# Optimization experiments

Hardware: AMD Instinct MI355X
Metric: run time of the kernel (lower is better)

Reference implementation:

```python
import jax, jax.numpy as jnp
import numpy as np

N_NODES = 200000
N_DEST = 8192
N_EDGE = 262144
E_TOTAL = 1000000
D_MEM = 128
D_FEAT = 128
D_EDGE = 64
D_TIME = 32
D_READ = 128
D_MSG = 128
D_AGG = 128
D_UPD = 128


def _glorot(key, shape):
    fan_in = shape[0]
    return jax.random.normal(key, shape, dtype=jnp.float32) * (1.0 / np.sqrt(fan_in))


def setup_inputs() -> dict:
    key = jax.random.key(0)
    ks = jax.random.split(key, 16)
    inp = {
        "node_memory": jax.random.normal(ks[0], (N_NODES, D_MEM), dtype=jnp.float32),
        "node_features": jax.random.normal(ks[1], (N_NODES, D_FEAT), dtype=jnp.float32),
        "edge_features": jax.random.normal(ks[2], (E_TOTAL, D_EDGE), dtype=jnp.float32),
        "time_encoding": jax.random.normal(ks[3], (N_EDGE, D_TIME), dtype=jnp.float32),
        "node_ids": jnp.arange(N_DEST, dtype=jnp.int64),
        "source_ids": jax.random.randint(ks[4], (N_EDGE,), 0, N_NODES, dtype=jnp.int64),
        "edge_ids": jax.random.randint(ks[5], (N_EDGE,), 0, E_TOTAL, dtype=jnp.int64),
        "dest_seg": jnp.sort(jax.random.randint(ks[6], (N_EDGE,), 0, N_DEST, dtype=jnp.int64)),
        # learned parameters
        "W_read": _glorot(ks[7], (D_MEM + D_FEAT, D_READ)),
        "b_read": jnp.zeros((D_READ,), dtype=jnp.float32),
        "W_msg": _glorot(ks[8], (D_READ + D_EDGE + D_TIME, D_MSG)),
        "b_msg": jnp.zeros((D_MSG,), dtype=jnp.float32),
        "W_agg": _glorot(ks[9], (D_READ + D_MSG, D_AGG)),
        "b_agg": jnp.zeros((D_AGG,), dtype=jnp.float32),
        "W_upd": _glorot(ks[10], (D_AGG + D_READ, D_UPD)),
        "b_upd": jnp.zeros((D_UPD,), dtype=jnp.float32),
        "W_write": _glorot(ks[11], (D_UPD, D_MEM)),
        "b_write": jnp.zeros((D_MEM,), dtype=jnp.float32),
    }
    return inp


def reference(node_memory, node_features, edge_features, time_encoding,
              node_ids, source_ids, edge_ids, dest_seg,
              W_read, b_read, W_msg, b_msg, W_agg, b_agg,
              W_upd, b_upd, W_write, b_write):
    n_dest = node_ids.shape[0]
    # source memory readout: gather + fuse(mem, feat) -> linear -> relu
    src_in = jnp.concatenate([node_memory[source_ids], node_features[source_ids]], axis=-1)
    src_read = jax.nn.relu(src_in @ W_read + b_read)                       # [E, D_READ]
    # message builder: fuse(source readout, edge feats, time enc) -> linear -> relu
    msg_in = jnp.concatenate([src_read, edge_features[edge_ids], time_encoding], axis=-1)
    msgs = jax.nn.relu(msg_in @ W_msg + b_msg)                             # [E, D_MSG]
    # ragged per-destination mean aggregation (replaces torch.split groups)
    msg_sum = jax.ops.segment_sum(msgs, dest_seg, num_segments=n_dest)     # [n_dest, D_MSG]
    cnt = jax.ops.segment_sum(jnp.ones((msgs.shape[0], 1), msgs.dtype), dest_seg, num_segments=n_dest)
    msg_mean = msg_sum / jnp.maximum(cnt, 1.0)
    # destination memory readout (shared with source readout: dest config is None)
    dst_in = jnp.concatenate([node_memory[node_ids], node_features[node_ids]], axis=-1)
    dst_read = jax.nn.relu(dst_in @ W_read + b_read)                       # [n_dest, D_READ]
    # aggregator: fuse(dest readout, mean messages) -> linear -> relu
    agg = jax.nn.relu(jnp.concatenate([dst_read, msg_mean], axis=-1) @ W_agg + b_agg)
    # memory updater: fuse(agg, dest readout) -> linear -> relu
    upd = jax.nn.relu(jnp.concatenate([agg, dst_read], axis=-1) @ W_upd + b_upd)
    # write-in: linear -> tanh, scatter back into node_memory
    write = jnp.tanh(upd @ W_write + b_write)                              # [n_dest, D_MEM]
    return node_memory.at[node_ids].set(write)
```

## Files before the change

kernel.cpp:

```cpp
#include <hip/hip_runtime.h>
#include <hip/hip_bf16.h>


typedef __bf16 bf16_t;
typedef __bf16 bf16x4 __attribute__((ext_vector_type(4)));
typedef __bf16 bf16x8 __attribute__((ext_vector_type(8)));
typedef float  f32x4  __attribute__((ext_vector_type(4)));

#define NNODES 200000
#define NDEST  8192
#define NEDGE  262144

__global__ void pack_weights_kernel(const float* __restrict__ Wr, const float* __restrict__ Wm,
                                    const float* __restrict__ Wa, const float* __restrict__ Wu,
                                    const float* __restrict__ Ww,
                                    bf16_t* __restrict__ Pr, bf16_t* __restrict__ Pm,
                                    bf16_t* __restrict__ Pa, bf16_t* __restrict__ Pu,
                                    bf16_t* __restrict__ Pw) {
    int p = blockIdx.x * 256 + threadIdx.x;
    const float* src; bf16_t* dst; int rel;
    if (p < 32768)       { src = Wr; dst = Pr; rel = p; }
    else if (p < 61440)  { src = Wm; dst = Pm; rel = p - 32768; }
    else if (p < 94208)  { src = Wa; dst = Pa; rel = p - 61440; }
    else if (p < 126976) { src = Wu; dst = Pu; rel = p - 94208; }
    else if (p < 143360) { src = Ww; dst = Pw; rel = p - 126976; }
    else return;
    int j    = rel & 7;
    int lane = (rel >> 3) & 63;
    int t    = rel >> 9;
    int nb   = t & 7;
    int kb   = t >> 3;
    int row  = kb * 32 + ((lane >> 4) << 3) + j;
    int col  = nb * 16 + (lane & 15);
    dst[rel] = (bf16_t)src[row * 128 + col];
}

__global__ __launch_bounds__(256, 2) void edge_kernel(
    const float* __restrict__ node_memory, const float* __restrict__ node_features,
    const float* __restrict__ edge_features, const float* __restrict__ time_enc,
    const int* __restrict__ source_ids, const int* __restrict__ edge_ids,
    const int* __restrict__ dest_seg,
    const bf16_t* __restrict__ Pr, const bf16_t* __restrict__ Pm,
    const float* __restrict__ b_read, const float* __restrict__ b_msg,
    float* __restrict__ msg_sum, float* __restrict__ out) {

    __shared__ __align__(16) bf16_t A1[64 * 264];
    __shared__ __align__(16) bf16_t A2[64 * 232];
    __shared__ int s_src[64], s_dst[64], s_eid[64];

    const int tid = threadIdx.x;
    const int e0  = blockIdx.x * 64;

    if (tid < 64) {
        s_src[tid] = source_ids[e0 + tid];
        s_dst[tid] = dest_seg[e0 + tid];
        s_eid[tid] = edge_ids[e0 + tid];
    }
    __syncthreads();

    #pragma unroll
    for (int i = 0; i < 16; ++i) {
        int c  = i * 256 + tid;
        int m  = c >> 6;
        int kc = (c & 63) << 2;
        int nrow = s_src[m];
        float4 v = (kc < 128)
            ? *(const float4*)(node_memory   + (size_t)nrow * 128 + kc)
            : *(const float4*)(node_features + (size_t)nrow * 128 + (kc - 128));
        bf16x4 pv = { (bf16_t)v.x, (bf16_t)v.y, (bf16_t)v.z, (bf16_t)v.w };
        *(bf16x4*)(A1 + m * 264 + kc) = pv;
    }
    #pragma unroll
    for (int i = 0; i < 4; ++i) {
        int c  = i * 256 + tid;
        int m  = c >> 4;
        int kc = (c & 15) << 2;
        float4 v = *(const float4*)(edge_features + (size_t)s_eid[m] * 64 + kc);
        bf16x4 pv = { (bf16_t)v.x, (bf16_t)v.y, (bf16_t)v.z, (bf16_t)v.w };
        *(bf16x4*)(A2 + m * 232 + 128 + kc) = pv;
    }
    #pragma unroll
    for (int i = 0; i < 2; ++i) {
        int c  = i * 256 + tid;
        int m  = c >> 3;
        int kc = (c & 7) << 2;
        float4 v = *(const float4*)(time_enc + (size_t)(e0 + m) * 32 + kc);
        bf16x4 pv = { (bf16_t)v.x, (bf16_t)v.y, (bf16_t)v.z, (bf16_t)v.w };
        *(bf16x4*)(A2 + m * 232 + 192 + kc) = pv;
    }
    __syncthreads();

    const int lane = tid & 63;
    const int w    = tid >> 6;
    const int quad = lane >> 4;
    const int lq   = lane & 15;
    const int n0   = w * 32;

    f32x4 acc[4][2] = {};
    #pragma unroll
    for (int kb = 0; kb < 8; ++kb) {
        bf16x8 b0 = *(const bf16x8*)(Pr + (((kb * 8 + (w * 2 + 0)) * 64 + lane) << 3));
        bf16x8 b1 = *(const bf16x8*)(Pr + (((kb * 8 + (w * 2 + 1)) * 64 + lane) << 3));
        #pragma unroll
        for (int mt = 0; mt < 4; ++mt) {
            bf16x8 a = *(const bf16x8*)(A1 + (mt * 16 + lq) * 264 + kb * 32 + quad * 8);
            acc[mt][0] = __builtin_amdgcn_mfma_f32_16x16x32_bf16(a, b0, acc[mt][0], 0, 0, 0);
            acc[mt][1] = __builtin_amdgcn_mfma_f32_16x16x32_bf16(a, b1, acc[mt][1], 0, 0, 0);
        }
    }
    {
        float bb0 = b_read[n0 + lq];
        float bb1 = b_read[n0 + 16 + lq];
        #pragma unroll
        for (int mt = 0; mt < 4; ++mt)
            #pragma unroll
            for (int nt = 0; nt < 2; ++nt) {
                float bb = nt ? bb1 : bb0;
                #pragma unroll
                for (int r = 0; r < 4; ++r) {
                    float v = fmaxf(acc[mt][nt][r] + bb, 0.f);
                    A2[(mt * 16 + quad * 4 + r) * 232 + (n0 + nt * 16 + lq)] = (bf16_t)v;
                }
            }
    }
    __syncthreads();

    f32x4 acc2[4][2] = {};
    #pragma unroll
    for (int kb = 0; kb < 7; ++kb) {
        bf16x8 b0 = *(const bf16x8*)(Pm + (((kb * 8 + (w * 2 + 0)) * 64 + lane) << 3));
        bf16x8 b1 = *(const bf16x8*)(Pm + (((kb * 8 + (w * 2 + 1)) * 64 + lane) << 3));
        #pragma unroll
        for (int mt = 0; mt < 4; ++mt) {
            bf16x8 a = *(const bf16x8*)(A2 + (mt * 16 + lq) * 232 + kb * 32 + quad * 8);
            acc2[mt][0] = __builtin_amdgcn_mfma_f32_16x16x32_bf16(a, b0, acc2[mt][0], 0, 0, 0);
            acc2[mt][1] = __builtin_amdgcn_mfma_f32_16x16x32_bf16(a, b1, acc2[mt][1], 0, 0, 0);
        }
    }
    float* Msg = (float*)A1;
    {
        float bb0 = b_msg[n0 + lq];
        float bb1 = b_msg[n0 + 16 + lq];
        #pragma unroll
        for (int mt = 0; mt < 4; ++mt)
            #pragma unroll
            for (int nt = 0; nt < 2; ++nt) {
                float bb = nt ? bb1 : bb0;
                #pragma unroll
                for (int r = 0; r < 4; ++r) {
                    float v = fmaxf(acc2[mt][nt][r] + bb, 0.f);
                    Msg[(mt * 16 + quad * 4 + r) * 132 + (n0 + nt * 16 + lq)] = v;
                }
            }
    }
    __syncthreads();

    if (tid < 128) {
        int cur = s_dst[0];
        float run = 0.f;
        for (int m = 0; m < 64; ++m) {
            int d = s_dst[m];
            if (d != cur) {
                atomicAdd(msg_sum + (size_t)cur * 128 + tid, run);
                run = 0.f; cur = d;
            }
            run += Msg[m * 132 + tid];
        }
        atomicAdd(msg_sum + (size_t)cur * 128 + tid, run);
    }

    {
        const float4* s4 = (const float4*)node_memory;
        float4* d4 = (float4*)out;
        const int total4 = (NNODES * 128) / 4;
        const int stride = gridDim.x * 256;
        for (int i = blockIdx.x * 256 + tid; i < total4; i += stride)
            d4[i] = s4[i];
    }
}

__global__ __launch_bounds__(256, 2) void dest_kernel(
    const float* __restrict__ node_memory, const float* __restrict__ node_features,
    const int* __restrict__ node_ids, const int* __restrict__ dest_seg,
    const bf16_t* __restrict__ Pr, const bf16_t* __restrict__ Pa,
    const bf16_t* __restrict__ Pu, const bf16_t* __restrict__ Pw,
    const float* __restrict__ b_read, const float* __restrict__ b_agg,
    const float* __restrict__ b_upd, const float* __restrict__ b_write,
    const float* __restrict__ msg_sum, float* __restrict__ out) {

    __shared__ __align__(16) bf16_t B1[32 * 264];
    __shared__ __align__(16) bf16_t B2[32 * 264];
    __shared__ int   s_nid[32];
    __shared__ int   s_lb[64];
    __shared__ float s_inv[32];

    const int tid = threadIdx.x;
    const int s0  = blockIdx.x * 32;

    if (tid < 32) s_nid[tid] = node_ids[s0 + tid];
    if (tid < 64) {
        int t = tid & 31, half = tid >> 5;
        int target = s0 + t + half;
        int lo = 0, hi = NEDGE;
        while (lo < hi) { int mid = (lo + hi) >> 1; if (dest_seg[mid] < target) lo = mid + 1; else hi = mid; }
        s_lb[tid] = lo;
    }
    __syncthreads();
    if (tid < 32) {
        int cnt = s_lb[tid + 32] - s_lb[tid];
        s_inv[tid] = 1.f / (float)(cnt > 1 ? cnt : 1);
    }
    #pragma unroll
    for (int i = 0; i < 8; ++i) {
        int c = i * 256 + tid; int m = c >> 6; int kc = (c & 63) << 2;
        int nrow = s_nid[m];
        float4 v = (kc < 128)
            ? *(const float4*)(node_memory   + (size_t)nrow * 128 + kc)
            : *(const float4*)(node_features + (size_t)nrow * 128 + (kc - 128));
        bf16x4 pv = { (bf16_t)v.x, (bf16_t)v.y, (bf16_t)v.z, (bf16_t)v.w };
        *(bf16x4*)(B1 + m * 264 + kc) = pv;
    }
    __syncthreads();
    #pragma unroll
    for (int i = 0; i < 4; ++i) {
        int c = i * 256 + tid; int m = c >> 5; int kc = (c & 31) << 2;
        float4 v = *(const float4*)(msg_sum + (size_t)(s0 + m) * 128 + kc);
        float inv = s_inv[m];
        bf16x4 pv = { (bf16_t)(v.x * inv), (bf16_t)(v.y * inv), (bf16_t)(v.z * inv), (bf16_t)(v.w * inv) };
        *(bf16x4*)(B2 + m * 264 + 128 + kc) = pv;
    }

    const int lane = tid & 63;
    const int w    = tid >> 6;
    const int quad = lane >> 4;
    const int lq   = lane & 15;
    const int n0   = w * 32;

    {
        f32x4 acc[2][2] = {};
        #pragma unroll
        for (int kb = 0; kb < 8; ++kb) {
            bf16x8 b0 = *(const bf16x8*)(Pr + (((kb * 8 + (w * 2 + 0)) * 64 + lane) << 3));
            bf16x8 b1 = *(const bf16x8*)(Pr + (((kb * 8 + (w * 2 + 1)) * 64 + lane) << 3));
            #pragma unroll
            for (int mt = 0; mt < 2; ++mt) {
                bf16x8 a = *(const bf16x8*)(B1 + (mt * 16 + lq) * 264 + kb * 32 + quad * 8);
                acc[mt][0] = __builtin_amdgcn_mfma_f32_16x16x32_bf16(a, b0, acc[mt][0], 0, 0, 0);
                acc[mt][1] = __builtin_amdgcn_mfma_f32_16x16x32_bf16(a, b1, acc[mt][1], 0, 0, 0);
            }
        }
        float bb0 = b_read[n0 + lq], bb1 = b_read[n0 + 16 + lq];
        #pragma unroll
        for (int mt = 0; mt < 2; ++mt)
            #pragma unroll
            for (int nt = 0; nt < 2; ++nt) {
                float bb = nt ? bb1 : bb0;
                #pragma unroll
                for (int r = 0; r < 4; ++r) {
                    float v = fmaxf(acc[mt][nt][r] + bb, 0.f);
                    B2[(mt * 16 + quad * 4 + r) * 264 + (n0 + nt * 16 + lq)] = (bf16_t)v;
                }
            }
    }
    __syncthreads();

    {
        f32x4 acc[2][2] = {};
        #pragma unroll
        for (int kb = 0; kb < 8; ++kb) {
            bf16x8 b0 = *(const bf16x8*)(Pa + (((kb * 8 + (w * 2 + 0)) * 64 + lane) << 3));
            bf16x8 b1 = *(const bf16x8*)(Pa + (((kb * 8 + (w * 2 + 1)) * 64 + lane) << 3));
            #pragma unroll
            for (int mt = 0; mt < 2; ++mt) {
                bf16x8 a = *(const bf16x8*)(B2 + (mt * 16 + lq) * 264 + kb * 32 + quad * 8);
                acc[mt][0] = __builtin_amdgcn_mfma_f32_16x16x32_bf16(a, b0, acc[mt][0], 0, 0, 0);
                acc[mt][1] = __builtin_amdgcn_mfma_f32_16x16x32_bf16(a, b1, acc[mt][1], 0, 0, 0);
            }
        }
        float bb0 = b_agg[n0 + lq], bb1 = b_agg[n0 + 16 + lq];
        #pragma unroll
        for (int mt = 0; mt < 2; ++mt)
            #pragma unroll
            for (int nt = 0; nt < 2; ++nt) {
                float bb = nt ? bb1 : bb0;
                #pragma unroll
                for (int r = 0; r < 4; ++r) {
                    float v = fmaxf(acc[mt][nt][r] + bb, 0.f);
                    B1[(mt * 16 + quad * 4 + r) * 264 + (n0 + nt * 16 + lq)] = (bf16_t)v;
                }
            }
    }
    __syncthreads();

    {
        f32x4 acc[2][2] = {};
        #pragma unroll
        for (int kb = 0; kb < 8; ++kb) {
            bf16x8 b0 = *(const bf16x8*)(Pu + (((kb * 8 + (w * 2 + 0)) * 64 + lane) << 3));
            bf16x8 b1 = *(const bf16x8*)(Pu + (((kb * 8 + (w * 2 + 1)) * 64 + lane) << 3));
            #pragma unroll
            for (int mt = 0; mt < 2; ++mt) {
                bf16x8 a = (kb < 4)
                    ? *(const bf16x8*)(B1 + (mt * 16 + lq) * 264 + kb * 32 + quad * 8)
                    : *(const bf16x8*)(B2 + (mt * 16 + lq) * 264 + (kb - 4) * 32 + quad * 8);
                acc[mt][0] = __builtin_amdgcn_mfma_f32_16x16x32_bf16(a, b0, acc[mt][0], 0, 0, 0);
                acc[mt][1] = __builtin_amdgcn_mfma_f32_16x16x32_bf16(a, b1, acc[mt][1], 0, 0, 0);
            }
        }
        float bb0 = b_upd[n0 + lq], bb1 = b_upd[n0 + 16 + lq];
        #pragma unroll
        for (int mt = 0; mt < 2; ++mt)
            #pragma unroll
            for (int nt = 0; nt < 2; ++nt) {
                float bb = nt ? bb1 : bb0;
                #pragma unroll
                for (int r = 0; r < 4; ++r) {
                    float v = fmaxf(acc[mt][nt][r] + bb, 0.f);
                    B1[(mt * 16 + quad * 4 + r) * 264 + 128 + (n0 + nt * 16 + lq)] = (bf16_t)v;
                }
            }
    }
    __syncthreads();

    {
        f32x4 acc[2][2] = {};
        #pragma unroll
        for (int kb = 0; kb < 4; ++kb) {
            bf16x8 b0 = *(const bf16x8*)(Pw + (((kb * 8 + (w * 2 + 0)) * 64 + lane) << 3));
            bf16x8 b1 = *(const bf16x8*)(Pw + (((kb * 8 + (w * 2 + 1)) * 64 + lane) << 3));
            #pragma unroll
            for (int mt = 0; mt < 2; ++mt) {
                bf16x8 a = *(const bf16x8*)(B1 + (mt * 16 + lq) * 264 + 128 + kb * 32 + quad * 8);
                acc[mt][0] = __builtin_amdgcn_mfma_f32_16x16x32_bf16(a, b0, acc[mt][0], 0, 0, 0);
                acc[mt][1] = __builtin_amdgcn_mfma_f32_16x16x32_bf16(a, b1, acc[mt][1], 0, 0, 0);
            }
        }
        float bb0 = b_write[n0 + lq], bb1 = b_write[n0 + 16 + lq];
        #pragma unroll
        for (int mt = 0; mt < 2; ++mt)
            #pragma unroll
            for (int nt = 0; nt < 2; ++nt) {
                float bb = nt ? bb1 : bb0;
                #pragma unroll
                for (int r = 0; r < 4; ++r) {
                    int row = mt * 16 + quad * 4 + r;
                    int col = n0 + nt * 16 + lq;
                    out[(size_t)s_nid[row] * 128 + col] = tanhf(acc[mt][nt][r] + bb);
                }
            }
    }
}

extern "C" void kernel_launch(void* const* d_in, const int* in_sizes, int n_in,
                              void* d_out, int out_size, void* d_ws, size_t ws_size,
                              hipStream_t stream) {
    const float* node_memory   = (const float*)d_in[0];
    const float* node_features = (const float*)d_in[1];
    const float* edge_features = (const float*)d_in[2];
    const float* time_enc      = (const float*)d_in[3];
    const int*   node_ids      = (const int*)d_in[4];
    const int*   source_ids    = (const int*)d_in[5];
    const int*   edge_ids      = (const int*)d_in[6];
    const int*   dest_seg      = (const int*)d_in[7];
    const float* W_read  = (const float*)d_in[8];
    const float* b_read  = (const float*)d_in[9];
    const float* W_msg   = (const float*)d_in[10];
    const float* b_msg   = (const float*)d_in[11];
    const float* W_agg   = (const float*)d_in[12];
    const float* b_agg   = (const float*)d_in[13];
    const float* W_upd   = (const float*)d_in[14];
    const float* b_upd   = (const float*)d_in[15];
    const float* W_write = (const float*)d_in[16];
    const float* b_write = (const float*)d_in[17];
    float* out = (float*)d_out;

    char* ws = (char*)d_ws;
    float*  msg_sum = (float*)(ws + 0);
    bf16_t* Pr = (bf16_t*)(ws + 4194304);
    bf16_t* Pm = (bf16_t*)(ws + 4194304 + 65536);
    bf16_t* Pa = (bf16_t*)(ws + 4194304 + 122880);
    bf16_t* Pu = (bf16_t*)(ws + 4194304 + 188416);
    bf16_t* Pw = (bf16_t*)(ws + 4194304 + 253952);

    hipMemsetAsync(msg_sum, 0, (size_t)NDEST * 128 * sizeof(float), stream);
    pack_weights_kernel<<<560, 256, 0, stream>>>(W_read, W_msg, W_agg, W_upd, W_write,
                                                 Pr, Pm, Pa, Pu, Pw);
    edge_kernel<<<NEDGE / 64, 256, 0, stream>>>(node_memory, node_features, edge_features,
                                                time_enc, source_ids, edge_ids, dest_seg,
                                                Pr, Pm, b_read, b_msg, msg_sum, out);
    dest_kernel<<<NDEST / 32, 256, 0, stream>>>(node_memory, node_features, node_ids, dest_seg,
                                                Pr, Pa, Pu, Pw, b_read, b_agg, b_upd, b_write,
                                                msg_sum, out);
}
```

Before: 606.9 us.

## Share LDS buffer in edge kernel, raise occupancy, count edges via atomics

The edge kernel merges its two LDS staging buffers into one, holding edge and time features in registers until the first GEMM finishes, and raises launch bounds to 4 blocks per CU. It also accumulates per-destination edge counts with atomics, which replaces the binary search over dest_seg in the dest kernel. The dest kernel now uses 16-row tiles for more blocks and higher occupancy, and swaps tanhf for an exp-based fast tanh. The trade-offs are extra barriers, extra atomics, lower per-block MFMA reuse in the dest kernel, and slightly different tanh accuracy.

Result: faster. 560.0 us (-7.7%).

```diff
diff --git a/kernel.cpp b/kernel.cpp
--- a/kernel.cpp
+++ b/kernel.cpp
@@ -10,6 +10,11 @@
 #define NNODES 200000
 #define NDEST  8192
 #define NEDGE  262144
+
+__device__ __forceinline__ float fast_tanh(float x) {
+    float e = __expf(2.f * x);
+    return 1.f - 2.f / (e + 1.f);
+}
 
 __global__ void pack_weights_kernel(const float* __restrict__ Wr, const float* __restrict__ Wm,
                                     const float* __restrict__ Wa, const float* __restrict__ Wu,
@@ -35,17 +40,16 @@
     dst[rel] = (bf16_t)src[row * 128 + col];
 }
 
-__global__ __launch_bounds__(256, 2) void edge_kernel(
+__global__ __launch_bounds__(256, 4) void edge_kernel(
     const float* __restrict__ node_memory, const float* __restrict__ node_features,
     const float* __restrict__ edge_features, const float* __restrict__ time_enc,
     const int* __restrict__ source_ids, const int* __restrict__ edge_ids,
     const int* __restrict__ dest_seg,
     const bf16_t* __restrict__ Pr, const bf16_t* __restrict__ Pm,
     const float* __restrict__ b_read, const float* __restrict__ b_msg,
-    float* __restrict__ msg_sum, float* __restrict__ out) {
-
-    __shared__ __align__(16) bf16_t A1[64 * 264];
-    __shared__ __align__(16) bf16_t A2[64 * 232];
+    float* __restrict__ msg_sum, float* __restrict__ cnt, float* __restrict__ out) {
+
+    __shared__ __align__(16) bf16_t S[64 * 264];
     __shared__ int s_src[64], s_dst[64], s_eid[64];
 
     const int tid = threadIdx.x;
@@ -57,6 +61,20 @@
         s_eid[tid] = edge_ids[e0 + tid];
     }
     __syncthreads();
+
+    bf16x4 r_e[4], r_t[2];
+    #pragma unroll
+    for (int i = 0; i < 4; ++i) {
+        int c = i * 256 + tid; int m = c >> 4; int kc = (c & 15) << 2;
+        float4 v = *(const float4*)(edge_features + (size_t)s_eid[m] * 64 + kc);
+        r_e[i] = bf16x4{ (bf16_t)v.x, (bf16_t)v.y, (bf16_t)v.z, (bf16_t)v.w };
+    }
+    #pragma unroll
+    for (int i = 0; i < 2; ++i) {
+        int c = i * 256 + tid; int m = c >> 3; int kc = (c & 7) << 2;
+        float4 v = *(const float4*)(time_enc + (size_t)(e0 + m) * 32 + kc);
+        r_t[i] = bf16x4{ (bf16_t)v.x, (bf16_t)v.y, (bf16_t)v.z, (bf16_t)v.w };
+    }
 
     #pragma unroll
     for (int i = 0; i < 16; ++i) {
@@ -67,26 +85,7 @@
         float4 v = (kc < 128)
             ? *(const float4*)(node_memory   + (size_t)nrow * 128 + kc)
             : *(const float4*)(node_features + (size_t)nrow * 128 + (kc - 128));
-        bf16x4 pv = { (bf16_t)v.x, (bf16_t)v.y, (bf16_t)v.z, (bf16_t)v.w };
-        *(bf16x4*)(A1 + m * 264 + kc) = pv;
-    }
-    #pragma unroll
-    for (int i = 0; i < 4; ++i) {
-        int c  = i * 256 + tid;
-        int m  = c >> 4;
-        int kc = (c & 15) << 2;
-        float4 v = *(const float4*)(edge_features + (size_t)s_eid[m] * 64 + kc);
-        bf16x4 pv = { (bf16_t)v.x, (bf16_t)v.y, (bf16_t)v.z, (bf16_t)v.w };
-        *(bf16x4*)(A2 + m * 232 + 128 + kc) = pv;
-    }
-    #pragma unroll
-    for (int i = 0; i < 2; ++i) {
-        int c  = i * 256 + tid;
-        int m  = c >> 3;
-        int kc = (c & 7) << 2;
-        float4 v = *(const float4*)(time_enc + (size_t)(e0 + m) * 32 + kc);
-        bf16x4 pv = { (bf16_t)v.x, (bf16_t)v.y, (bf16_t)v.z, (bf16_t)v.w };
-        *(bf16x4*)(A2 + m * 232 + 192 + kc) = pv;
+        *(bf16x4*)(S + m * 264 + kc) = bf16x4{ (bf16_t)v.x, (bf16_t)v.y, (bf16_t)v.z, (bf16_t)v.w };
     }
     __syncthreads();
 
@@ -103,10 +102,22 @@
         bf16x8 b1 = *(const bf16x8*)(Pr + (((kb * 8 + (w * 2 + 1)) * 64 + lane) << 3));
         #pragma unroll
         for (int mt = 0; mt < 4; ++mt) {
-            bf16x8 a = *(const bf16x8*)(A1 + (mt * 16 + lq) * 264 + kb * 32 + quad * 8);
+            bf16x8 a = *(const bf16x8*)(S + (mt * 16 + lq) * 264 + kb * 32 + quad * 8);
             acc[mt][0] = __builtin_amdgcn_mfma_f32_16x16x32_bf16(a, b0, acc[mt][0], 0, 0, 0);
             acc[mt][1] = __builtin_amdgcn_mfma_f32_16x16x32_bf16(a, b1, acc[mt][1], 0, 0, 0);
         }
+    }
+    __syncthreads();
+
+    #pragma unroll
+    for (int i = 0; i < 4; ++i) {
+        int c = i * 256 + tid; int m = c >> 4; int kc = (c & 15) << 2;
+        *(bf16x4*)(S + m * 264 + 128 + kc) = r_e[i];
+    }
+    #pragma unroll
+    for (int i = 0; i < 2; ++i) {
+        int c = i * 256 + tid; int m = c >> 3; int kc = (c & 7) << 2;
+        *(bf16x4*)(S + m * 264 + 192 + kc) = r_t[i];
     }
     {
         float bb0 = b_read[n0 + lq];
@@ -119,7 +130,7 @@
                 #pragma unroll
                 for (int r = 0; r < 4; ++r) {
                     float v = fmaxf(acc[mt][nt][r] + bb, 0.f);
-                    A2[(mt * 16 + quad * 4 + r) * 232 + (n0 + nt * 16 + lq)] = (bf16_t)v;
+                    S[(mt * 16 + quad * 4 + r) * 264 + (n0 + nt * 16 + lq)] = (bf16_t)v;
                 }
             }
     }
@@ -132,12 +143,14 @@
         bf16x8 b1 = *(const bf16x8*)(Pm + (((kb * 8 + (w * 2 + 1)) * 64 + lane) << 3));
         #pragma unroll
         for (int mt = 0; mt < 4; ++mt) {
-            bf16x8 a = *(const bf16x8*)(A2 + (mt * 16 + lq) * 232 + kb * 32 + quad * 8);
+            bf16x8 a = *(const bf16x8*)(S + (mt * 16 + lq) * 264 + kb * 32 + quad * 8);
             acc2[mt][0] = __builtin_amdgcn_mfma_f32_16x16x32_bf16(a, b0, acc2[mt][0], 0, 0, 0);
             acc2[mt][1] = __builtin_amdgcn_mfma_f32_16x16x32_bf16(a, b1, acc2[mt][1], 0, 0, 0);
         }
     }
-    float* Msg = (float*)A1;
+    __syncthreads();
+
+    float* Msg = (float*)S;
     {
         float bb0 = b_msg[n0 + lq];
         float bb1 = b_msg[n0 + 16 + lq];
@@ -167,6 +180,15 @@
             run += Msg[m * 132 + tid];
         }
         atomicAdd(msg_sum + (size_t)cur * 128 + tid, run);
+    } else if (tid == 128) {
+        int cur = s_dst[0];
+        float run = 0.f;
+        for (int m = 0; m < 64; ++m) {
+            int d = s_dst[m];
+            if (d != cur) { atomicAdd(cnt + cur, run); run = 0.f; cur = d; }
+            run += 1.f;
+        }
+        atomicAdd(cnt + cur, run);
     }
 
     {
@@ -179,56 +201,48 @@
     }
 }
 
-__global__ __launch_bounds__(256, 2) void dest_kernel(
+__global__ __launch_bounds__(256, 4) void dest_kernel(
     const float* __restrict__ node_memory, const float* __restrict__ node_features,
-    const int* __restrict__ node_ids, const int* __restrict__ dest_seg,
+    const int* __restrict__ node_ids,
     const bf16_t* __restrict__ Pr, const bf16_t* __restrict__ Pa,
     const bf16_t* __restrict__ Pu, const bf16_t* __restrict__ Pw,
     const float* __restrict__ b_read, const float* __restrict__ b_agg,
     const float* __restrict__ b_upd, const float* __restrict__ b_write,
-    const float* __restrict__ msg_sum, float* __restrict__ out) {
-
-    __shared__ __align__(16) bf16_t B1[32 * 264];
-    __shared__ __align__(16) bf16_t B2[32 * 264];
-    __shared__ int   s_nid[32];
-    __shared__ int   s_lb[64];
-    __shared__ float s_inv[32];
+    const float* __restrict__ msg_sum, const float* __restrict__ cnt,
+    float* __restrict__ out) {
+
+    __shared__ __align__(16) bf16_t B1[16 * 264];
+    __shared__ __align__(16) bf16_t B2[16 * 264];
+    __shared__ int   s_nid[16];
+    __shared__ float s_inv[16];
 
     const int tid = threadIdx.x;
-    const int s0  = blockIdx.x * 32;
-
-    if (tid < 32) s_nid[tid] = node_ids[s0 + tid];
-    if (tid < 64) {
-        int t = tid & 31, half = tid >> 5;
-        int target = s0 + t + half;
-        int lo = 0, hi = NEDGE;
-        while (lo < hi) { int mid = (lo + hi) >> 1; if (dest_seg[mid] < target) lo = mid + 1; else hi = mid; }
-        s_lb[tid] = lo;
-    }
-    __syncthreads();
-    if (tid < 32) {
-        int cnt = s_lb[tid + 32] - s_lb[tid];
-        s_inv[tid] = 1.f / (float)(cnt > 1 ? cnt : 1);
-    }
-    #pragma unroll
-    for (int i = 0; i < 8; ++i) {
+    const int s0  = blockIdx.x * 16;
+
+    if (tid < 16) {
+        s_nid[tid] = node_ids[s0 + tid];
+        s_inv[tid] = 1.f / fmaxf(cnt[s0 + tid], 1.f);
+    }
+    __syncthreads();
+
+    #pragma unroll
+    for (int i = 0; i < 4; ++i) {
         int c = i * 256 + tid; int m = c >> 6; int kc = (c & 63) << 2;
         int nrow = s_nid[m];
         float4 v = (kc < 128)
             ? *(const float4*)(node_memory   + (size_t)nrow * 128 + kc)
             : *(const float4*)(node_features + (size_t)nrow * 128 + (kc - 128));
-        bf16x4 pv = { (bf16_t)v.x, (bf16_t)v.y, (bf16_t)v.z, (bf16_t)v.w };
-        *(bf16x4*)(B1 + m * 264 + kc) = pv;
-    }
-    __syncthreads();
-    #pragma unroll
-    for (int i = 0; i < 4; ++i) {
+        *(bf16x4*)(B1 + m * 264 + kc) = bf16x4{ (bf16_t)v.x, (bf16_t)v.y, (bf16_t)v.z, (bf16_t)v.w };
+    }
+    #pragma unroll
+    for (int i = 0; i < 2; ++i) {
         int c = i * 256 + tid; int m = c >> 5; int kc = (c & 31) << 2;
         float4 v = *(const float4*)(msg_sum + (size_t)(s0 + m) * 128 + kc);
         float inv = s_inv[m];
-        bf16x4 pv = { (bf16_t)(v.x * inv), (bf16_t)(v.y * inv), (bf16_t)(v.z * inv), (bf16_t)(v.w * inv) };
-        *(bf16x4*)(B2 + m * 264 + 128 + kc) = pv;
-    }
+        *(bf16x4*)(B2 + m * 264 + 128 + kc) =
+            bf16x4{ (bf16_t)(v.x * inv), (bf16_t)(v.y * inv), (bf16_t)(v.z * inv), (bf16_t)(v.w * inv) };
+    }
+    __syncthreads();
 
     const int lane = tid & 63;
     const int w    = tid >> 6;
@@ -237,117 +251,97 @@
     const int n0   = w * 32;
 
     {
-        f32x4 acc[2][2] = {};
+        f32x4 acc[2] = {};
         #pragma unroll
         for (int kb = 0; kb < 8; ++kb) {
             bf16x8 b0 = *(const bf16x8*)(Pr + (((kb * 8 + (w * 2 + 0)) * 64 + lane) << 3));
             bf16x8 b1 = *(const bf16x8*)(Pr + (((kb * 8 + (w * 2 + 1)) * 64 + lane) << 3));
-            #pragma unroll
-            for (int mt = 0; mt < 2; ++mt) {
-                bf16x8 a = *(const bf16x8*)(B1 + (mt * 16 + lq) * 264 + kb * 32 + quad * 8);
-                acc[mt][0] = __builtin_amdgcn_mfma_f32_16x16x32_bf16(a, b0, acc[mt][0], 0, 0, 0);
-                acc[mt][1] = __builtin_amdgcn_mfma_f32_16x16x32_bf16(a, b1, acc[mt][1], 0, 0, 0);
-            }
+            bf16x8 a  = *(const bf16x8*)(B1 + lq * 264 + kb * 32 + quad * 8);
+            acc[0] = __builtin_amdgcn_mfma_f32_16x16x32_bf16(a, b0, acc[0], 0, 0, 0);
+            acc[1] = __builtin_amdgcn_mfma_f32_16x16x32_bf16(a, b1, acc[1], 0, 0, 0);
         }
         float bb0 = b_read[n0 + lq], bb1 = b_read[n0 + 16 + lq];
         #pragma unroll
-        for (int mt = 0; mt < 2; ++mt)
-            #pragma unroll
-            for (int nt = 0; nt < 2; ++nt) {
-                float bb = nt ? bb1 : bb0;
-                #pragma unroll
-                for (int r = 0; r < 4; ++r) {
-                    float v = fmaxf(acc[mt][nt][r] + bb, 0.f);
-                    B2[(mt * 16 + quad * 4 + r) * 264 + (n0 + nt * 16 + lq)] = (bf16_t)v;
-                }
-            }
-    }
-    __syncthreads();
-
-    {
-        f32x4 acc[2][2] = {};
+        for (int nt = 0; nt < 2; ++nt) {
+            float bb = nt ? bb1 : bb0;
+            #pragma unroll
+            for (int r = 0; r < 4; ++r) {
+                float v = fmaxf(acc[nt][r] + bb, 0.f);
+                B2[(quad * 4 + r) * 264 + (n0 + nt * 16 + lq)] = (bf16_t)v;
+            }
+        }
+    }
+    __syncthreads();
+
+    {
+        f32x4 acc[2] = {};
         #pragma unroll
         for (int kb = 0; kb < 8; ++kb) {
             bf16x8 b0 = *(const bf16x8*)(Pa + (((kb * 8 + (w * 2 + 0)) * 64 + lane) << 3));
             bf16x8 b1 = *(const bf16x8*)(Pa + (((kb * 8 + (w * 2 + 1)) * 64 + lane) << 3));
-            #pragma unroll
-            for (int mt = 0; mt < 2; ++mt) {
-                bf16x8 a = *(const bf16x8*)(B2 + (mt * 16 + lq) * 264 + kb * 32 + quad * 8);
-                acc[mt][0] = __builtin_amdgcn_mfma_f32_16x16x32_bf16(a, b0, acc[mt][0], 0, 0, 0);
-                acc[mt][1] = __builtin_amdgcn_mfma_f32_16x16x32_bf16(a, b1, acc[mt][1], 0, 0, 0);
-            }
+            bf16x8 a  = *(const bf16x8*)(B2 + lq * 264 + kb * 32 + quad * 8);
+            acc[0] = __builtin_amdgcn_mfma_f32_16x16x32_bf16(a, b0, acc[0], 0, 0, 0);
+            acc[1] = __builtin_amdgcn_mfma_f32_16x16x32_bf16(a, b1, acc[1], 0, 0, 0);
         }
         float bb0 = b_agg[n0 + lq], bb1 = b_agg[n0 + 16 + lq];
         #pragma unroll
-        for (int mt = 0; mt < 2; ++mt)
-            #pragma unroll
-            for (int nt = 0; nt < 2; ++nt) {
-                float bb = nt ? bb1 : bb0;
-                #pragma unroll
-                for (int r = 0; r < 4; ++r) {
-                    float v = fmaxf(acc[mt][nt][r] + bb, 0.f);
-                    B1[(mt * 16 + quad * 4 + r) * 264 + (n0 + nt * 16 + lq)] = (bf16_t)v;
-                }
-            }
-    }
-    __syncthreads();
-
-    {
-        f32x4 acc[2][2] = {};
+        for (int nt = 0; nt < 2; ++nt) {
+            float bb = nt ? bb1 : bb0;
+            #pragma unroll
+            for (int r = 0; r < 4; ++r) {
+                float v = fmaxf(acc[nt][r] + bb, 0.f);
+                B1[(quad * 4 + r) * 264 + (n0 + nt * 16 + lq)] = (bf16_t)v;
+            }
+        }
+    }
+    __syncthreads();
+
+    {
+        f32x4 acc[2] = {};
         #pragma unroll
         for (int kb = 0; kb < 8; ++kb) {
             bf16x8 b0 = *(const bf16x8*)(Pu + (((kb * 8 + (w * 2 + 0)) * 64 + lane) << 3));
             bf16x8 b1 = *(const bf16x8*)(Pu + (((kb * 8 + (w * 2 + 1)) * 64 + lane) << 3));
-            #pragma unroll
-            for (int mt = 0; mt < 2; ++mt) {
-                bf16x8 a = (kb < 4)
-                    ? *(const bf16x8*)(B1 + (mt * 16 + lq) * 264 + kb * 32 + quad * 8)
-                    : *(const bf16x8*)(B2 + (mt * 16 + lq) * 264 + (kb - 4) * 32 + quad * 8);
-                acc[mt][0] = __builtin_amdgcn_mfma_f32_16x16x32_bf16(a, b0, acc[mt][0], 0, 0, 0);
-                acc[mt][1] = __builtin_amdgcn_mfma_f32_16x16x32_bf16(a, b1, acc[mt][1], 0, 0, 0);
-            }
+            bf16x8 a  = (kb < 4)
+                ? *(const bf16x8*)(B1 + lq * 264 + kb * 32 + quad * 8)
+                : *(const bf16x8*)(B2 + lq * 264 + (kb - 4) * 32 + quad * 8);
+            acc[0] = __builtin_amdgcn_mfma_f32_16x16x32_bf16(a, b0, acc[0], 0, 0, 0);
+            acc[1] = __builtin_amdgcn_mfma_f32_16x16x32_bf16(a, b1, acc[1], 0, 0, 0);
         }
         float bb0 = b_upd[n0 + lq], bb1 = b_upd[n0 + 16 + lq];
         #pragma unroll
-        for (int mt = 0; mt < 2; ++mt)
-            #pragma unroll
-            for (int nt = 0; nt < 2; ++nt) {
-                float bb = nt ? bb1 : bb0;
-                #pragma unroll
-                for (int r = 0; r < 4; ++r) {
-                    float v = fmaxf(acc[mt][nt][r] + bb, 0.f);
-                    B1[(mt * 16 + quad * 4 + r) * 264 + 128 + (n0 + nt * 16 + lq)] = (bf16_t)v;
-                }
-            }
-    }
-    __syncthreads();
-
-    {
-        f32x4 acc[2][2] = {};
+        for (int nt = 0; nt < 2; ++nt) {
+            float bb = nt ? bb1 : bb0;
+            #pragma unroll
+            for (int r = 0; r < 4; ++r) {
+                float v = fmaxf(acc[nt][r] + bb, 0.f);
+                B1[(quad * 4 + r) * 264 + 128 + (n0 + nt * 16 + lq)] = (bf16_t)v;
+            }
+        }
+    }
+    __syncthreads();
+
+    {
+        f32x4 acc[2] = {};
         #pragma unroll
         for (int kb = 0; kb < 4; ++kb) {
             bf16x8 b0 = *(const bf16x8*)(Pw + (((kb * 8 + (w * 2 + 0)) * 64 + lane) << 3));
             bf16x8 b1 = *(const bf16x8*)(Pw + (((kb * 8 + (w * 2 + 1)) * 64 + lane) << 3));
-            #pragma unroll
-            for (int mt = 0; mt < 2; ++mt) {
-                bf16x8 a = *(const bf16x8*)(B1 + (mt * 16 + lq) * 264 + 128 + kb * 32 + quad * 8);
-                acc[mt][0] = __builtin_amdgcn_mfma_f32_16x16x32_bf16(a, b0, acc[mt][0], 0, 0, 0);
-                acc[mt][1] = __builtin_amdgcn_mfma_f32_16x16x32_bf16(a, b1, acc[mt][1], 0, 0, 0);
-            }
+            bf16x8 a  = *(const bf16x8*)(B1 + lq * 264 + 128 + kb * 32 + quad * 8);
+            acc[0] = __builtin_amdgcn_mfma_f32_16x16x32_bf16(a, b0, acc[0], 0, 0, 0);
+            acc[1] = __builtin_amdgcn_mfma_f32_16x16x32_bf16(a, b1, acc[1], 0, 0, 0);
         }
         float bb0 = b_write[n0 + lq], bb1 = b_write[n0 + 16 + lq];
         #pragma unroll
-        for (int mt = 0; mt < 2; ++mt)
-            #pragma unroll
-            for (int nt = 0; nt < 2; ++nt) {
-                float bb = nt ? bb1 : bb0;
-                #pragma unroll
-                for (int r = 0; r < 4; ++r) {
-                    int row = mt * 16 + quad * 4 + r;
-                    int col = n0 + nt * 16 + lq;
-                    out[(size_t)s_nid[row] * 128 + col] = tanhf(acc[mt][nt][r] + bb);
-                }
-            }
+        for (int nt = 0; nt < 2; ++nt) {
+            float bb = nt ? bb1 : bb0;
+            #pragma unroll
+            for (int r = 0; r < 4; ++r) {
+                int row = quad * 4 + r;
+                int col = n0 + nt * 16 + lq;
+                out[(size_t)s_nid[row] * 128 + col] = fast_tanh(acc[nt][r] + bb);
+            }
+        }
     }
 }
 
@@ -358,10 +352,10 @@
     const float* node_features = (const float*)d_in[1];
     const float* edge_features = (const float*)d_in[2];
     const float* time_enc      = (const float*)d_in[3];
-    const int*   node_ids      = (const int*)d_in[4];
     const int*   source_ids    = (const int*)d_in[5];
     const int*   edge_ids      = (const int*)d_in[6];
     const int*   dest_seg      = (const int*)d_in[7];
+    const int*   node_ids      = (const int*)d_in[4];
     const float* W_read  = (const float*)d_in[8];
     const float* b_read  = (const float*)d_in[9];
     const float* W_msg   = (const float*)d_in[10];
@@ -376,19 +370,20 @@
 
     char* ws = (char*)d_ws;
     float*  msg_sum = (float*)(ws + 0);
-    bf16_t* Pr = (bf16_t*)(ws + 4194304);
-    bf16_t* Pm = (bf16_t*)(ws + 4194304 + 65536);
-    bf16_t* Pa = (bf16_t*)(ws + 4194304 + 122880);
-    bf16_t* Pu = (bf16_t*)(ws + 4194304 + 188416);
-    bf16_t* Pw = (bf16_t*)(ws + 4194304 + 253952);
-
-    hipMemsetAsync(msg_sum, 0, (size_t)NDEST * 128 * sizeof(float), stream);
+    float*  cnt     = (float*)(ws + 4194304);
+    bf16_t* Pr = (bf16_t*)(ws + 4227072);
+    bf16_t* Pm = (bf16_t*)(ws + 4292608);
+    bf16_t* Pa = (bf16_t*)(ws + 4349952);
+    bf16_t* Pu = (bf16_t*)(ws + 4415488);
+    bf16_t* Pw = (bf16_t*)(ws + 4481024);
+
+    hipMemsetAsync(msg_sum, 0, 4194304 + 32768, stream);
     pack_weights_kernel<<<560, 256, 0, stream>>>(W_read, W_msg, W_agg, W_upd, W_write,
                                                  Pr, Pm, Pa, Pu, Pw);
     edge_kernel<<<NEDGE / 64, 256, 0, stream>>>(node_memory, node_features, edge_features,
                                                 time_enc, source_ids, edge_ids, dest_seg,
-                                                Pr, Pm, b_read, b_msg, msg_sum, out);
-    dest_kernel<<<NDEST / 32, 256, 0, stream>>>(node_memory, node_features, node_ids, dest_seg,
+                                                Pr, Pm, b_read, b_msg, msg_sum, cnt, out);
+    dest_kernel<<<NDEST / 16, 256, 0, stream>>>(node_memory, node_features, node_ids,
                                                 Pr, Pa, Pu, Pw, b_read, b_agg, b_upd, b_write,
-                                                msg_sum, out);
-}
+                                                msg_sum, cnt, out);
+}
```
